# Performance work log

Measured on AMD Instinct MI355X. Metric: run time of the kernel, lower is better.

Reference implementation:

```python
import jax, jax.numpy as jnp
import numpy as np
from jax import lax

V, E, NL, NS, DC, EX = 32000, 1024, 4, 16, 4, 2
DI = EX * E          # 2048 inner dim
DTR = E // 16        # 64 dt_rank
BSZ, L = 2, 512
EPS = 1e-5


def setup_inputs() -> dict:
    key = jax.random.key(0)
    ks = jax.random.split(key, 12)
    s = 0.02
    emb = jax.random.normal(ks[0], (V, E), jnp.float32) * s
    ln_w = jnp.ones((NL, E), jnp.float32)
    ln_b = jnp.zeros((NL, E), jnp.float32)
    in_proj_w = jax.random.normal(ks[1], (NL, 2 * DI, E), jnp.float32) * s
    conv_w = jax.random.normal(ks[2], (NL, DI, DC), jnp.float32) * 0.1
    conv_b = jnp.zeros((NL, DI), jnp.float32)
    x_proj_w = jax.random.normal(ks[3], (NL, DTR + 2 * NS, DI), jnp.float32) * s
    dt_proj_w = jax.random.normal(ks[4], (NL, DI, DTR), jnp.float32) * s
    dt_proj_b = jax.random.normal(ks[5], (NL, DI), jnp.float32) * 0.1
    # canonical S4D-real init: A[d,n] = n+1  ->  A_log = log(A)
    A_log = jnp.log(jnp.tile(jnp.arange(1, NS + 1, dtype=jnp.float32)[None, None, :], (NL, DI, 1)))
    D_param = jnp.ones((NL, DI), jnp.float32)
    out_proj_w = jax.random.normal(ks[6], (NL, E, DI), jnp.float32) * s
    fln_w = jnp.ones((E,), jnp.float32)
    fln_b = jnp.zeros((E,), jnp.float32)
    input_ids = jax.random.randint(ks[7], (BSZ, L), 0, V, jnp.int64)
    targets = jax.random.randint(ks[8], (BSZ, L), 0, V, jnp.int64)
    return dict(input_ids=input_ids, targets=targets, emb=emb, ln_w=ln_w, ln_b=ln_b,
                in_proj_w=in_proj_w, conv_w=conv_w, conv_b=conv_b, x_proj_w=x_proj_w,
                dt_proj_w=dt_proj_w, dt_proj_b=dt_proj_b, A_log=A_log, D_param=D_param,
                out_proj_w=out_proj_w, fln_w=fln_w, fln_b=fln_b)


def _layer_norm(x, w, b):
    mu = x.mean(-1, keepdims=True)
    var = ((x - mu) ** 2).mean(-1, keepdims=True)
    return (x - mu) * lax.rsqrt(var + EPS) * w + b


def _mamba_block(x, in_w, cw, cb, xw, dtw, dtb, a_log, d_par, ow):
    # x: (B,L,E)
    xz = jnp.einsum('ble,fe->blf', x, in_w)          # (B,L,2*DI)
    u, res = jnp.split(xz, 2, axis=-1)               # each (B,L,DI)
    # causal depthwise conv1d, kernel width DC (left pad DC-1)
    u_pad = jnp.pad(u, ((0, 0), (DC - 1, 0), (0, 0)))
    u_conv = sum(cw[:, k] * u_pad[:, k:k + u.shape[1], :] for k in range(DC))
    u = jax.nn.silu(u_conv + cb)
    x_dbl = jnp.einsum('bld,fd->blf', u, xw)         # (B,L,DTR+2*NS)
    dt = x_dbl[..., :DTR]
    Bm = x_dbl[..., DTR:DTR + NS]                    # (B,L,NS)
    Cm = x_dbl[..., DTR + NS:]                       # (B,L,NS)
    delta = jax.nn.softplus(jnp.einsum('blr,dr->bld', dt, dtw) + dtb)  # (B,L,DI)
    A = -jnp.exp(a_log)                              # (DI,NS)
    dA = jnp.exp(delta[..., None] * A)               # (B,L,DI,NS)
    dBu = delta[..., None] * Bm[:, :, None, :] * u[..., None]

    def step(h, inp):
        dA_t, dBu_t, C_t = inp
        h = dA_t * h + dBu_t                         # (B,DI,NS)
        y = jnp.einsum('bdn,bn->bd', h, C_t)
        return h, y

    h0 = jnp.zeros((x.shape[0], DI, NS), x.dtype)
    _, ys = lax.scan(step, h0, (dA.transpose(1, 0, 2, 3), dBu.transpose(1, 0, 2, 3), Cm.transpose(1, 0, 2)))
    y = ys.transpose(1, 0, 2) + u * d_par            # (B,L,DI)
    y = y * jax.nn.silu(res)
    return jnp.einsum('bld,ed->ble', y, ow)


def reference(input_ids, targets, emb, ln_w, ln_b, in_proj_w, conv_w, conv_b,
              x_proj_w, dt_proj_w, dt_proj_b, A_log, D_param, out_proj_w, fln_w, fln_b):
    x = emb[input_ids]                               # (B,L,E)
    for l in range(NL):
        h = _layer_norm(x, ln_w[l], ln_b[l])
        h = _mamba_block(h, in_proj_w[l], conv_w[l], conv_b[l], x_proj_w[l],
                         dt_proj_w[l], dt_proj_b[l], A_log[l], D_param[l], out_proj_w[l])
        x = x + h
    x = _layer_norm(x, fln_w, fln_b)
    logits = jnp.einsum('ble,ve->blv', x, emb)       # tied lm_head
    logp = jax.nn.log_softmax(logits, axis=-1)
    valid = targets != -1
    safe_t = jnp.where(valid, targets, 0)
    nll = -jnp.take_along_axis(logp, safe_t[..., None], axis=-1)[..., 0]
    loss = jnp.where(valid, nll, 0.0).mean()
    return logits, loss
```

## Files before the change

### kernel.cpp

```cpp
#include <hip/hip_runtime.h>
#include <cstdint>
#include <cstddef>

#define L_SEQ 512
#define NBATCH 2
#define NTOK 1024
#define E_DIM 1024
#define V_DIM 32000
#define DI_DIM 2048
#define NS_DIM 16
#define DTR_DIM 64
#define DC_DIM 4
#define NL_DIM 4
#define NC 8
#define LC (L_SEQ / NC)
#define CB_LOG 250

typedef __bf16 bf16;
typedef __bf16 bf16x8 __attribute__((ext_vector_type(8)));
typedef __bf16 bf16x4 __attribute__((ext_vector_type(4)));
typedef float  f32x4  __attribute__((ext_vector_type(4)));

__device__ __forceinline__ void gload_lds16(const void* g, void* l)
{
    __builtin_amdgcn_global_load_lds((const __attribute__((address_space(1))) uint32_t*)g,
                                     (__attribute__((address_space(3))) uint32_t*)l, 16, 0, 0);
}

__device__ __forceinline__ float softplusf(float z)
{
    return fmaxf(z, 0.0f) + log1pf(expf(-fabsf(z)));
}

__global__ void cast_f32_to_bf16(const float* __restrict__ in, bf16* __restrict__ out, int n4)
{
    int stride = gridDim.x * blockDim.x;
    for (int i = blockIdx.x * blockDim.x + threadIdx.x; i < n4; i += stride) {
        f32x4 v = ((const f32x4*)in)[i];
        bf16x4 o;
        o[0] = (bf16)v[0]; o[1] = (bf16)v[1]; o[2] = (bf16)v[2]; o[3] = (bf16)v[3];
        ((bf16x4*)out)[i] = o;
    }
}

__global__ void cast3_kernel(const float* __restrict__ a, bf16* __restrict__ oa, int na4,
                             const float* __restrict__ b, bf16* __restrict__ ob, int nb4,
                             const float* __restrict__ c, bf16* __restrict__ oc, int nc4)
{
    int stride = gridDim.x * blockDim.x;
    int tot = na4 + nb4 + nc4;
    for (int i = blockIdx.x * blockDim.x + threadIdx.x; i < tot; i += stride) {
        const float* src; bf16* dst; int k = i;
        if (k < na4) { src = a; dst = oa; }
        else if ((k -= na4) < nb4) { src = b; dst = ob; }
        else { k -= nb4; src = c; dst = oc; }
        f32x4 v = ((const f32x4*)src)[k];
        bf16x4 o;
        o[0] = (bf16)v[0]; o[1] = (bf16)v[1]; o[2] = (bf16)v[2]; o[3] = (bf16)v[3];
        ((bf16x4*)dst)[k] = o;
    }
}

__global__ void embed_kernel(const int* __restrict__ ids, const float* __restrict__ emb,
                             float* __restrict__ x)
{
    int t = blockIdx.x;
    int id = ids[t];
    ((f32x4*)(x + (size_t)t * E_DIM))[threadIdx.x] =
        ((const f32x4*)(emb + (size_t)id * E_DIM))[threadIdx.x];
}

__global__ void ln_kernel(const float* __restrict__ x, const float* __restrict__ w,
                          const float* __restrict__ b, bf16* __restrict__ out)
{
    int t = blockIdx.x;
    int tid = threadIdx.x;
    f32x4 v = ((const f32x4*)(x + (size_t)t * E_DIM))[tid];
    float s  = v[0] + v[1] + v[2] + v[3];
    float sq = v[0]*v[0] + v[1]*v[1] + v[2]*v[2] + v[3]*v[3];
#pragma unroll
    for (int off = 1; off < 64; off <<= 1) { s += __shfl_xor(s, off); sq += __shfl_xor(sq, off); }
    __shared__ float ps[4], pq[4];
    if ((tid & 63) == 0) { ps[tid >> 6] = s; pq[tid >> 6] = sq; }
    __syncthreads();
    float S  = ps[0] + ps[1] + ps[2] + ps[3];
    float SQ = pq[0] + pq[1] + pq[2] + pq[3];
    float mu  = S * (1.0f / E_DIM);
    float var = SQ * (1.0f / E_DIM) - mu * mu;
    float rs  = rsqrtf(var + 1e-5f);
    f32x4 wv = ((const f32x4*)w)[tid];
    f32x4 bv = ((const f32x4*)b)[tid];
    bf16x4 o;
#pragma unroll
    for (int i = 0; i < 4; ++i) o[i] = (bf16)((v[i] - mu) * rs * wv[i] + bv[i]);
    ((bf16x4*)(out + (size_t)t * E_DIM))[tid] = o;
}

template<int BM, int BN, int MODE>
__global__ __launch_bounds__(256) void gemm_bt(const bf16* __restrict__ A, const bf16* __restrict__ B,
                                               void* __restrict__ Cv, int K,
                                               int lda, int ldb, int ldc,
                                               const float* __restrict__ bias,
                                               float* __restrict__ Pm, float* __restrict__ Ps,
                                               int RB, int CB, int CBpad)
{
    int pid = blockIdx.x;
    int xcd = pid & 7;
    int j   = pid >> 3;
    int cpx = CBpad >> 3;
    int rb  = j % RB;
    int cb  = xcd * cpx + j / RB;
    if (cb >= CB) return;

    __shared__ __align__(16) bf16 As[BM * 32];
    __shared__ __align__(16) bf16 Bs[BN * 32];
    int tid  = threadIdx.x;
    int lane = tid & 63;
    int wid  = tid >> 6;
    int wr = wid >> 1, wc = wid & 1;
    int li = lane & 15, lg = lane >> 4;
    const bf16* Ablk = A + (size_t)(rb * BM) * lda;
    const bf16* Bblk = B + (size_t)(cb * BN) * ldb;
    constexpr int MR  = BM / 32;
    constexpr int NR  = BN / 32;
    constexpr int TOT = (BM + BN) * 4;
    f32x4 acc[MR][NR] = {};
    for (int k0 = 0; k0 < K; k0 += 32) {
        __syncthreads();
#pragma unroll
        for (int it = 0; it < TOT / 256; ++it) {
            int wbase = it * 256 + wid * 64;
            int idx   = wbase + lane;
            if (wbase < BM * 4) {
                int row = idx >> 2, seg = idx & 3;
                gload_lds16(Ablk + (size_t)row * lda + k0 + seg * 8, As + (size_t)wbase * 8);
            } else {
                int bb  = wbase - BM * 4;
                int bi  = bb + lane;
                int row = bi >> 2, seg = bi & 3;
                gload_lds16(Bblk + (size_t)row * ldb + k0 + seg * 8, Bs + (size_t)bb * 8);
            }
        }
        __syncthreads();
        bf16x8 af[MR], bfr[NR];
#pragma unroll
        for (int m = 0; m < MR; ++m) af[m]  = *(const bf16x8*)&As[(wr * (BM/2) + m * 16 + li) * 32 + lg * 8];
#pragma unroll
        for (int n = 0; n < NR; ++n) bfr[n] = *(const bf16x8*)&Bs[(wc * (BN/2) + n * 16 + li) * 32 + lg * 8];
#pragma unroll
        for (int m = 0; m < MR; ++m)
#pragma unroll
            for (int n = 0; n < NR; ++n)
                acc[m][n] = __builtin_amdgcn_mfma_f32_16x16x32_bf16(af[m], bfr[n], acc[m][n], 0, 0, 0);
    }
    int row0 = rb * BM + wr * (BM/2);
    int col0 = cb * BN + wc * (BN/2);
    float* Cf = (float*)Cv;
    bf16*  Cb = (bf16*)Cv;
#pragma unroll
    for (int m = 0; m < MR; ++m) {
#pragma unroll
        for (int n = 0; n < NR; ++n) {
            int r = row0 + m * 16 + lg * 4;
            int c = col0 + n * 16 + li;
#pragma unroll
            for (int q = 0; q < 4; ++q) {
                float v = acc[m][n][q];
                if (MODE == 0 || MODE == 3) {
                    Cf[(size_t)(r + q) * ldc + c] = v;
                } else if (MODE == 1) {
                    float* cp = Cf + (size_t)(r + q) * ldc + c;
                    *cp = v + *cp;
                } else if (MODE == 2) {
                    Cb[(size_t)(r + q) * ldc + c] = (bf16)softplusf(v + bias[c]);
                } else if (MODE == 4) {
                    Cb[(size_t)(r + q) * ldc + c] = (bf16)v;
                }
            }
        }
    }
    if constexpr (MODE == 3) {
#pragma unroll
        for (int m = 0; m < MR; ++m) {
#pragma unroll
            for (int q = 0; q < 4; ++q) {
                float mx = acc[m][0][q];
#pragma unroll
                for (int n = 1; n < NR; ++n) mx = fmaxf(mx, acc[m][n][q]);
#pragma unroll
                for (int off = 1; off < 16; off <<= 1) mx = fmaxf(mx, __shfl_xor(mx, off));
                float sv = 0.0f;
#pragma unroll
                for (int n = 0; n < NR; ++n) sv += __expf(acc[m][n][q] - mx);
#pragma unroll
                for (int off = 1; off < 16; off <<= 1) sv += __shfl_xor(sv, off);
                if (li == 0) {
                    size_t r = (size_t)(row0 + m * 16 + lg * 4 + q);
                    Pm[r * 512 + cb * 2 + wc] = mx;
                    Ps[r * 512 + cb * 2 + wc] = sv;
                }
            }
        }
    }
}

template<int BM, int BN, int MODE>
static void launch_gemm(const bf16* A, const bf16* B, void* C, int M, int N, int K,
                        int lda, int ldb, int ldc, const float* bias,
                        float* Pm, float* Ps, hipStream_t stream)
{
    int RB = M / BM;
    int CB = (N + BN - 1) / BN;
    int CBpad = (CB + 7) & ~7;
    gemm_bt<BM, BN, MODE><<<RB * CBpad, 256, 0, stream>>>(A, B, C, K, lda, ldb, ldc,
                                                          bias, Pm, Ps, RB, CB, CBpad);
}

__global__ __launch_bounds__(256) void cxk_kernel(
        const bf16* __restrict__ xz, const float* __restrict__ cw,
        const float* __restrict__ cb, const float* __restrict__ xw,
        float* __restrict__ xdbl, bf16* __restrict__ dt_bf, bf16* __restrict__ u_bf)
{
    int t0  = blockIdx.x * 4;
    int bb  = t0 >> 9;
    int tid = threadIdx.x;
    int f   = tid & 127;
    int ks  = tid >> 7;
    __shared__ __align__(16) float sxz[7][256];
    __shared__ __align__(16) float su[4][256];
    __shared__ float pacc[4][128];
    float acc[4] = {0, 0, 0, 0};
    for (int kc = 0; kc < DI_DIM; kc += 256) {
        __syncthreads();
        if (tid < 224) {
            int row = tid >> 5, c8 = (tid & 31) * 8;
            int tr = t0 - 3 + row;
            float vals[8] = {0, 0, 0, 0, 0, 0, 0, 0};
            if (tr >= bb * L_SEQ) {
                bf16x8 v = *(const bf16x8*)&xz[(size_t)tr * (2 * DI_DIM) + kc + c8];
#pragma unroll
                for (int jj = 0; jj < 8; ++jj) vals[jj] = (float)v[jj];
            }
#pragma unroll
            for (int jj = 0; jj < 8; ++jj) sxz[row][c8 + jj] = vals[jj];
        }
        __syncthreads();
        {
            int c = tid;
            const float* cwp = cw + (size_t)(kc + c) * DC_DIM;
            float w0 = cwp[0], w1 = cwp[1], w2 = cwp[2], w3 = cwp[3];
            float bs = cb[kc + c];
#pragma unroll
            for (int tt = 0; tt < 4; ++tt) {
                float a = bs + w0 * sxz[tt][c] + w1 * sxz[tt + 1][c]
                             + w2 * sxz[tt + 2][c] + w3 * sxz[tt + 3][c];
                float uo = a / (1.0f + __expf(-a));
                su[tt][c] = uo;
                u_bf[(size_t)(t0 + tt) * DI_DIM + kc + c] = (bf16)uo;
            }
        }
        __syncthreads();
        if (f < 96) {
            int kb = ks * 128;
            for (int kk = kb; kk < kb + 128; kk += 4) {
                f32x4 wv = *(const f32x4*)&xw[(size_t)f * DI_DIM + kc + kk];
#pragma unroll
                for (int tt = 0; tt < 4; ++tt) {
                    f32x4 uv = *(f32x4*)&su[tt][kk];
                    acc[tt] += wv[0]*uv[0] + wv[1]*uv[1] + wv[2]*uv[2] + wv[3]*uv[3];
                }
            }
        }
    }
    if (ks == 1 && f < 96) {
#pragma unroll
        for (int tt = 0; tt < 4; ++tt) pacc[tt][f] = acc[tt];
    }
    __syncthreads();
    if (ks == 0 && f < 96) {
#pragma unroll
        for (int tt = 0; tt < 4; ++tt) {
            float v = acc[tt] + pacc[tt][f];
            xdbl[(size_t)(t0 + tt) * 96 + f] = v;
            if (f < 64) dt_bf[(size_t)(t0 + tt) * DTR_DIM + f] = (bf16)v;
        }
    }
}

__global__ __launch_bounds__(256) void scan_phase_a(
        const bf16* __restrict__ delta, const float* __restrict__ xdbl,
        const bf16* __restrict__ u_bf, const float* __restrict__ A_log,
        float* __restrict__ Pbuf, float* __restrict__ Sbuf)
{
    int tid = threadIdx.x;
    int c   = blockIdx.x & (NC - 1);
    int dblk= (blockIdx.x >> 3) & 127;
    int b   = blockIdx.x >> 10;
    int d0  = dblk << 4;
    int n = tid & 15, dl = tid >> 4;
    int d = d0 + dl;
    float Ac = -expf(A_log[(size_t)d * NS_DIM + n]);
    float h = 0.0f, P = 1.0f;
    __shared__ float s_dlt[32][16], s_u[32][16], s_B[32][16];
    int tt0 = tid >> 4, cc = tid & 15;
    int tbase = b * L_SEQ + c * LC;
    for (int t0 = 0; t0 < LC; t0 += 32) {
        __syncthreads();
#pragma unroll
        for (int jj = 0; jj < 2; ++jj) {
            int tt = jj * 16 + tt0;
            size_t trow = (size_t)(tbase + t0 + tt);
            s_dlt[tt][cc] = (float)delta[trow * DI_DIM + d0 + cc];
            s_u[tt][cc]   = (float)u_bf[trow * DI_DIM + d0 + cc];
            s_B[tt][cc]   = xdbl[trow * 96 + 64 + cc];
        }
        __syncthreads();
#pragma unroll
        for (int t = 0; t < 32; ++t) {
            float dlt = s_dlt[t][dl];
            float dA  = __expf(dlt * Ac);
            h = fmaf(dA, h, dlt * s_B[t][n] * s_u[t][dl]);
            P *= dA;
        }
    }
    size_t oi = (((size_t)(b * NC + c) * DI_DIM) + d) * NS_DIM + n;
    Pbuf[oi] = P;
    Sbuf[oi] = h;
}

__global__ void scan_combine(const float* __restrict__ Pbuf, const float* __restrict__ Sbuf,
                             float* __restrict__ Hstart)
{
    int i  = blockIdx.x * 256 + threadIdx.x;
    int b  = i >> 15;
    int dn = i & 32767;
    float h = 0.0f;
#pragma unroll
    for (int c = 0; c < NC; ++c) {
        size_t oi = ((size_t)(b * NC + c) * (DI_DIM * NS_DIM)) + dn;
        Hstart[oi] = h;
        h = fmaf(Pbuf[oi], h, Sbuf[oi]);
    }
}

__global__ __launch_bounds__(256) void scan_phase_c(
        const bf16* __restrict__ delta, const float* __restrict__ xdbl,
        const bf16* __restrict__ u_bf, const bf16* __restrict__ xz,
        const float* __restrict__ A_log, const float* __restrict__ D_par,
        const float* __restrict__ Hstart, bf16* __restrict__ y)
{
    int tid = threadIdx.x;
    int c   = blockIdx.x & (NC - 1);
    int dblk= (blockIdx.x >> 3) & 127;
    int b   = blockIdx.x >> 10;
    int d0  = dblk << 4;
    int n = tid & 15, dl = tid >> 4;
    int d = d0 + dl;
    float Ac = -expf(A_log[(size_t)d * NS_DIM + n]);
    float Dp = D_par[d];
    float h = Hstart[(((size_t)(b * NC + c) * DI_DIM) + d) * NS_DIM + n];
    __shared__ float s_dlt[32][16], s_u[32][16], s_res[32][16], s_B[32][16], s_C[32][16];
    __shared__ bf16  s_y[32][16];
    int tt0 = tid >> 4, cc = tid & 15;
    int tbase = b * L_SEQ + c * LC;
    for (int t0 = 0; t0 < LC; t0 += 32) {
        __syncthreads();
#pragma unroll
        for (int jj = 0; jj < 2; ++jj) {
            int tt = jj * 16 + tt0;
            size_t trow = (size_t)(tbase + t0 + tt);
            s_dlt[tt][cc] = (float)delta[trow * DI_DIM + d0 + cc];
            s_u[tt][cc]   = (float)u_bf[trow * DI_DIM + d0 + cc];
            s_res[tt][cc] = (float)xz[trow * (2 * DI_DIM) + DI_DIM + d0 + cc];
            s_B[tt][cc]   = xdbl[trow * 96 + 64 + cc];
            s_C[tt][cc]   = xdbl[trow * 96 + 80 + cc];
        }
        __syncthreads();
#pragma unroll
        for (int t = 0; t < 32; ++t) {
            float dlt = s_dlt[t][dl];
            float uu  = s_u[t][dl];
            float dA  = __expf(dlt * Ac);
            float dBu = dlt * s_B[t][n] * uu;
            h = fmaf(dA, h, dBu);
            float yp = h * s_C[t][n];
            yp += __shfl_xor(yp, 1);
            yp += __shfl_xor(yp, 2);
            yp += __shfl_xor(yp, 4);
            yp += __shfl_xor(yp, 8);
            if (n == 0) {
                float res = s_res[t][dl];
                float yv  = fmaf(uu, Dp, yp) * (res / (1.0f + __expf(-res)));
                s_y[t][dl] = (bf16)yv;
            }
        }
        __syncthreads();
#pragma unroll
        for (int jj = 0; jj < 2; ++jj) {
            int tt = jj * 16 + tt0;
            size_t trow = (size_t)(tbase + t0 + tt);
            y[trow * DI_DIM + d0 + cc] = s_y[tt][cc];
        }
    }
}

__global__ void lse_fin_kernel(const float* __restrict__ Pm, const float* __restrict__ Ps,
                               const float* __restrict__ logits, const int* __restrict__ targets,
                               float* __restrict__ lossp)
{
    int t = blockIdx.x, tid = threadIdx.x;
    float m = -1e30f, s = 0.0f;
    for (int i = tid; i < 2 * CB_LOG; i += 256) {
        float mo = Pm[(size_t)t * 512 + i], so = Ps[(size_t)t * 512 + i];
        float nm = fmaxf(m, mo);
        s = s * __expf(m - nm) + so * __expf(mo - nm);
        m = nm;
    }
#pragma unroll
    for (int off = 1; off < 64; off <<= 1) {
        float mo = __shfl_xor(m, off), so = __shfl_xor(s, off);
        float nm = fmaxf(m, mo);
        s = s * __expf(m - nm) + so * __expf(mo - nm);
        m = nm;
    }
    __shared__ float pm[4], ps2[4];
    if ((tid & 63) == 0) { pm[tid >> 6] = m; ps2[tid >> 6] = s; }
    __syncthreads();
    if (tid == 0) {
        float M = fmaxf(fmaxf(pm[0], pm[1]), fmaxf(pm[2], pm[3]));
        float S = ps2[0] * __expf(pm[0] - M) + ps2[1] * __expf(pm[1] - M)
                + ps2[2] * __expf(pm[2] - M) + ps2[3] * __expf(pm[3] - M);
        int tg = targets[t];
        if (tg >= 0) {
            float v = (M + logf(S)) - logits[(size_t)t * V_DIM + tg];
            atomicAdd(lossp, v * (1.0f / NTOK));
        }
    }
}

extern "C" void kernel_launch(void* const* d_in, const int* in_sizes, int n_in,
                              void* d_out, int out_size, void* d_ws, size_t ws_size,
                              hipStream_t stream)
{
    const int*   ids   = (const int*)d_in[0];
    const int*   tgt   = (const int*)d_in[1];
    const float* emb   = (const float*)d_in[2];
    const float* ln_w  = (const float*)d_in[3];
    const float* ln_b  = (const float*)d_in[4];
    const float* inw   = (const float*)d_in[5];
    const float* convw = (const float*)d_in[6];
    const float* convb = (const float*)d_in[7];
    const float* xw    = (const float*)d_in[8];
    const float* dtw   = (const float*)d_in[9];
    const float* dtb   = (const float*)d_in[10];
    const float* alog  = (const float*)d_in[11];
    const float* dpar  = (const float*)d_in[12];
    const float* outw  = (const float*)d_in[13];
    const float* flnw  = (const float*)d_in[14];
    const float* flnb  = (const float*)d_in[15];
    float* logits = (float*)d_out;
    float* lossp  = logits + (size_t)NTOK * V_DIM;

    char* wsp = (char*)d_ws;
    size_t off = 0;
    auto alloc = [&](size_t bytes) -> void* {
        void* p = wsp + off;
        off += (bytes + 255) & ~(size_t)255;
        return p;
    };
    bf16*  emb_bf  = (bf16*)alloc((size_t)V_DIM * E_DIM * 2);
    bf16*  winl    = (bf16*)alloc((size_t)2 * DI_DIM * E_DIM * 2);
    bf16*  woutl   = (bf16*)alloc((size_t)E_DIM * DI_DIM * 2);
    bf16*  wdtl    = (bf16*)alloc((size_t)DI_DIM * DTR_DIM * 2);
    float* x       = (float*)alloc((size_t)NTOK * E_DIM * 4);
    bf16*  h_bf    = (bf16*)alloc((size_t)NTOK * E_DIM * 2);
    bf16*  xzb     = (bf16*)alloc((size_t)NTOK * 2 * DI_DIM * 2);
    bf16*  u_bf    = (bf16*)alloc((size_t)NTOK * DI_DIM * 2);
    float* xdbl    = (float*)alloc((size_t)NTOK * 96 * 4);
    bf16*  dt_bf   = (bf16*)alloc((size_t)NTOK * DTR_DIM * 2);
    bf16*  deltab  = (bf16*)alloc((size_t)NTOK * DI_DIM * 2);
    bf16*  y_bf    = (bf16*)alloc((size_t)NTOK * DI_DIM * 2);
    bf16*  xf_bf   = (bf16*)alloc((size_t)NTOK * E_DIM * 2);
    float* Pbuf    = (float*)alloc((size_t)NBATCH * NC * DI_DIM * NS_DIM * 4);
    float* Sbuf    = (float*)alloc((size_t)NBATCH * NC * DI_DIM * NS_DIM * 4);
    float* Hstart  = (float*)alloc((size_t)NBATCH * NC * DI_DIM * NS_DIM * 4);
    float* Pm      = (float*)alloc((size_t)NTOK * 512 * 4);
    float* Ps      = (float*)alloc((size_t)NTOK * 512 * 4);
    if (off > ws_size) return;

    hipMemsetAsync(lossp, 0, sizeof(float), stream);
    {
        int n4 = (int)((size_t)V_DIM * E_DIM / 4);
        cast_f32_to_bf16<<<4096, 256, 0, stream>>>(emb, emb_bf, n4);
    }
    embed_kernel<<<NTOK, 256, 0, stream>>>(ids, emb, x);

    for (int l = 0; l < NL_DIM; ++l) {
        cast3_kernel<<<2048, 256, 0, stream>>>(
            inw  + (size_t)l * 2 * DI_DIM * E_DIM, winl,  (int)((size_t)2 * DI_DIM * E_DIM / 4),
            outw + (size_t)l * E_DIM * DI_DIM,     woutl, (int)((size_t)E_DIM * DI_DIM / 4),
            dtw  + (size_t)l * DI_DIM * DTR_DIM,   wdtl,  (int)((size_t)DI_DIM * DTR_DIM / 4));

        ln_kernel<<<NTOK, 256, 0, stream>>>(x, ln_w + l * E_DIM, ln_b + l * E_DIM, h_bf);
        launch_gemm<128, 64, 4>(h_bf, winl, xzb, NTOK, 2 * DI_DIM, E_DIM,
                                E_DIM, E_DIM, 2 * DI_DIM, nullptr, nullptr, nullptr, stream);
        cxk_kernel<<<NTOK / 4, 256, 0, stream>>>(
            xzb, convw + (size_t)l * DI_DIM * DC_DIM, convb + (size_t)l * DI_DIM,
            xw + (size_t)l * 96 * DI_DIM, xdbl, dt_bf, u_bf);
        launch_gemm<64, 64, 2>(dt_bf, wdtl, deltab, NTOK, DI_DIM, DTR_DIM,
                               DTR_DIM, DTR_DIM, DI_DIM, dtb + (size_t)l * DI_DIM,
                               nullptr, nullptr, stream);
        scan_phase_a<<<NBATCH * (DI_DIM / 16) * NC, 256, 0, stream>>>(
            deltab, xdbl, u_bf, alog + (size_t)l * DI_DIM * NS_DIM, Pbuf, Sbuf);
        scan_combine<<<NBATCH * DI_DIM * NS_DIM / 256, 256, 0, stream>>>(Pbuf, Sbuf, Hstart);
        scan_phase_c<<<NBATCH * (DI_DIM / 16) * NC, 256, 0, stream>>>(
            deltab, xdbl, u_bf, xzb, alog + (size_t)l * DI_DIM * NS_DIM,
            dpar + (size_t)l * DI_DIM, Hstart, y_bf);
        launch_gemm<64, 64, 1>(y_bf, woutl, x, NTOK, E_DIM, DI_DIM,
                               DI_DIM, DI_DIM, E_DIM, nullptr, nullptr, nullptr, stream);
    }
    ln_kernel<<<NTOK, 256, 0, stream>>>(x, flnw, flnb, xf_bf);
    launch_gemm<128, 128, 3>(xf_bf, emb_bf, logits, NTOK, V_DIM, E_DIM,
                             E_DIM, E_DIM, V_DIM, nullptr, Pm, Ps, stream);
    lse_fin_kernel<<<NTOK, 256, 0, stream>>>(Pm, Ps, logits, tgt, lossp);
}
```

Measured before the change: 884.9 us.

## Unfuse softmax partials from LM-head GEMM and halve tokens per conv block

```diff
diff --git a/kernel.cpp b/kernel.cpp
--- a/kernel.cpp
+++ b/kernel.cpp
@@ -14,7 +14,6 @@
 #define NL_DIM 4
 #define NC 8
 #define LC (L_SEQ / NC)
-#define CB_LOG 250
 
 typedef __bf16 bf16;
 typedef __bf16 bf16x8 __attribute__((ext_vector_type(8)));
@@ -101,7 +100,6 @@
                                                void* __restrict__ Cv, int K,
                                                int lda, int ldb, int ldc,
                                                const float* __restrict__ bias,
-                                               float* __restrict__ Pm, float* __restrict__ Ps,
                                                int RB, int CB, int CBpad)
 {
     int pid = blockIdx.x;
@@ -166,7 +164,7 @@
 #pragma unroll
             for (int q = 0; q < 4; ++q) {
                 float v = acc[m][n][q];
-                if (MODE == 0 || MODE == 3) {
+                if (MODE == 0) {
                     Cf[(size_t)(r + q) * ldc + c] = v;
                 } else if (MODE == 1) {
                     float* cp = Cf + (size_t)(r + q) * ldc + c;
@@ -179,41 +177,17 @@
             }
         }
     }
-    if constexpr (MODE == 3) {
-#pragma unroll
-        for (int m = 0; m < MR; ++m) {
-#pragma unroll
-            for (int q = 0; q < 4; ++q) {
-                float mx = acc[m][0][q];
-#pragma unroll
-                for (int n = 1; n < NR; ++n) mx = fmaxf(mx, acc[m][n][q]);
-#pragma unroll
-                for (int off = 1; off < 16; off <<= 1) mx = fmaxf(mx, __shfl_xor(mx, off));
-                float sv = 0.0f;
-#pragma unroll
-                for (int n = 0; n < NR; ++n) sv += __expf(acc[m][n][q] - mx);
-#pragma unroll
-                for (int off = 1; off < 16; off <<= 1) sv += __shfl_xor(sv, off);
-                if (li == 0) {
-                    size_t r = (size_t)(row0 + m * 16 + lg * 4 + q);
-                    Pm[r * 512 + cb * 2 + wc] = mx;
-                    Ps[r * 512 + cb * 2 + wc] = sv;
-                }
-            }
-        }
-    }
 }
 
 template<int BM, int BN, int MODE>
 static void launch_gemm(const bf16* A, const bf16* B, void* C, int M, int N, int K,
-                        int lda, int ldb, int ldc, const float* bias,
-                        float* Pm, float* Ps, hipStream_t stream)
+                        int lda, int ldb, int ldc, const float* bias, hipStream_t stream)
 {
     int RB = M / BM;
     int CB = (N + BN - 1) / BN;
     int CBpad = (CB + 7) & ~7;
     gemm_bt<BM, BN, MODE><<<RB * CBpad, 256, 0, stream>>>(A, B, C, K, lda, ldb, ldc,
-                                                          bias, Pm, Ps, RB, CB, CBpad);
+                                                          bias, RB, CB, CBpad);
 }
 
 __global__ __launch_bounds__(256) void cxk_kernel(
@@ -221,28 +195,31 @@
         const float* __restrict__ cb, const float* __restrict__ xw,
         float* __restrict__ xdbl, bf16* __restrict__ dt_bf, bf16* __restrict__ u_bf)
 {
-    int t0  = blockIdx.x * 4;
+    int t0  = blockIdx.x * 2;
     int bb  = t0 >> 9;
     int tid = threadIdx.x;
     int f   = tid & 127;
     int ks  = tid >> 7;
-    __shared__ __align__(16) float sxz[7][256];
-    __shared__ __align__(16) float su[4][256];
-    __shared__ float pacc[4][128];
-    float acc[4] = {0, 0, 0, 0};
+    __shared__ __align__(16) float sxz[5][256];
+    __shared__ __align__(16) float su[2][256];
+    __shared__ float pacc[2][128];
+    float acc[2] = {0, 0};
     for (int kc = 0; kc < DI_DIM; kc += 256) {
         __syncthreads();
-        if (tid < 224) {
-            int row = tid >> 5, c8 = (tid & 31) * 8;
-            int tr = t0 - 3 + row;
-            float vals[8] = {0, 0, 0, 0, 0, 0, 0, 0};
-            if (tr >= bb * L_SEQ) {
-                bf16x8 v = *(const bf16x8*)&xz[(size_t)tr * (2 * DI_DIM) + kc + c8];
-#pragma unroll
-                for (int jj = 0; jj < 8; ++jj) vals[jj] = (float)v[jj];
+#pragma unroll
+        for (int it = 0; it < 2; ++it) {
+            int idx = it * 256 + tid;
+            if (idx < 320) {
+                int row = idx >> 6, c4 = (idx & 63) * 4;
+                int tr = t0 - 3 + row;
+                float v0 = 0, v1 = 0, v2 = 0, v3 = 0;
+                if (tr >= bb * L_SEQ) {
+                    bf16x4 v = *(const bf16x4*)&xz[(size_t)tr * (2 * DI_DIM) + kc + c4];
+                    v0 = (float)v[0]; v1 = (float)v[1]; v2 = (float)v[2]; v3 = (float)v[3];
+                }
+                sxz[row][c4] = v0; sxz[row][c4 + 1] = v1;
+                sxz[row][c4 + 2] = v2; sxz[row][c4 + 3] = v3;
             }
-#pragma unroll
-            for (int jj = 0; jj < 8; ++jj) sxz[row][c8 + jj] = vals[jj];
         }
         __syncthreads();
         {
@@ -251,7 +228,7 @@
             float w0 = cwp[0], w1 = cwp[1], w2 = cwp[2], w3 = cwp[3];
             float bs = cb[kc + c];
 #pragma unroll
-            for (int tt = 0; tt < 4; ++tt) {
+            for (int tt = 0; tt < 2; ++tt) {
                 float a = bs + w0 * sxz[tt][c] + w1 * sxz[tt + 1][c]
                              + w2 * sxz[tt + 2][c] + w3 * sxz[tt + 3][c];
                 float uo = a / (1.0f + __expf(-a));
@@ -265,7 +242,7 @@
             for (int kk = kb; kk < kb + 128; kk += 4) {
                 f32x4 wv = *(const f32x4*)&xw[(size_t)f * DI_DIM + kc + kk];
 #pragma unroll
-                for (int tt = 0; tt < 4; ++tt) {
+                for (int tt = 0; tt < 2; ++tt) {
                     f32x4 uv = *(f32x4*)&su[tt][kk];
                     acc[tt] += wv[0]*uv[0] + wv[1]*uv[1] + wv[2]*uv[2] + wv[3]*uv[3];
                 }
@@ -274,12 +251,12 @@
     }
     if (ks == 1 && f < 96) {
 #pragma unroll
-        for (int tt = 0; tt < 4; ++tt) pacc[tt][f] = acc[tt];
+        for (int tt = 0; tt < 2; ++tt) pacc[tt][f] = acc[tt];
     }
     __syncthreads();
     if (ks == 0 && f < 96) {
 #pragma unroll
-        for (int tt = 0; tt < 4; ++tt) {
+        for (int tt = 0; tt < 2; ++tt) {
             float v = acc[tt] + pacc[tt][f];
             xdbl[(size_t)(t0 + tt) * 96 + f] = v;
             if (f < 64) dt_bf[(size_t)(t0 + tt) * DTR_DIM + f] = (bf16)v;
@@ -404,17 +381,17 @@
     }
 }
 
-__global__ void lse_fin_kernel(const float* __restrict__ Pm, const float* __restrict__ Ps,
-                               const float* __restrict__ logits, const int* __restrict__ targets,
+__global__ void lse_nll_kernel(const float* __restrict__ logits, const int* __restrict__ targets,
                                float* __restrict__ lossp)
 {
     int t = blockIdx.x, tid = threadIdx.x;
+    const f32x4* row = (const f32x4*)(logits + (size_t)t * V_DIM);
     float m = -1e30f, s = 0.0f;
-    for (int i = tid; i < 2 * CB_LOG; i += 256) {
-        float mo = Pm[(size_t)t * 512 + i], so = Ps[(size_t)t * 512 + i];
-        float nm = fmaxf(m, mo);
-        s = s * __expf(m - nm) + so * __expf(mo - nm);
-        m = nm;
+    for (int i = tid; i < V_DIM / 4; i += 256) {
+        f32x4 v = row[i];
+        float m4 = fmaxf(fmaxf(v[0], v[1]), fmaxf(v[2], v[3]));
+        if (m4 > m) { s *= __expf(m - m4); m = m4; }
+        s += __expf(v[0] - m) + __expf(v[1] - m) + __expf(v[2] - m) + __expf(v[3] - m);
     }
 #pragma unroll
     for (int off = 1; off < 64; off <<= 1) {
@@ -484,8 +461,6 @@
     float* Pbuf    = (float*)alloc((size_t)NBATCH * NC * DI_DIM * NS_DIM * 4);
     float* Sbuf    = (float*)alloc((size_t)NBATCH * NC * DI_DIM * NS_DIM * 4);
     float* Hstart  = (float*)alloc((size_t)NBATCH * NC * DI_DIM * NS_DIM * 4);
-    float* Pm      = (float*)alloc((size_t)NTOK * 512 * 4);
-    float* Ps      = (float*)alloc((size_t)NTOK * 512 * 4);
     if (off > ws_size) return;
 
     hipMemsetAsync(lossp, 0, sizeof(float), stream);
@@ -503,13 +478,12 @@
 
         ln_kernel<<<NTOK, 256, 0, stream>>>(x, ln_w + l * E_DIM, ln_b + l * E_DIM, h_bf);
         launch_gemm<128, 64, 4>(h_bf, winl, xzb, NTOK, 2 * DI_DIM, E_DIM,
-                                E_DIM, E_DIM, 2 * DI_DIM, nullptr, nullptr, nullptr, stream);
-        cxk_kernel<<<NTOK / 4, 256, 0, stream>>>(
+                                E_DIM, E_DIM, 2 * DI_DIM, nullptr, stream);
+        cxk_kernel<<<NTOK / 2, 256, 0, stream>>>(
             xzb, convw + (size_t)l * DI_DIM * DC_DIM, convb + (size_t)l * DI_DIM,
             xw + (size_t)l * 96 * DI_DIM, xdbl, dt_bf, u_bf);
         launch_gemm<64, 64, 2>(dt_bf, wdtl, deltab, NTOK, DI_DIM, DTR_DIM,
-                               DTR_DIM, DTR_DIM, DI_DIM, dtb + (size_t)l * DI_DIM,
-                               nullptr, nullptr, stream);
+                               DTR_DIM, DTR_DIM, DI_DIM, dtb + (size_t)l * DI_DIM, stream);
         scan_phase_a<<<NBATCH * (DI_DIM / 16) * NC, 256, 0, stream>>>(
             deltab, xdbl, u_bf, alog + (size_t)l * DI_DIM * NS_DIM, Pbuf, Sbuf);
         scan_combine<<<NBATCH * DI_DIM * NS_DIM / 256, 256, 0, stream>>>(Pbuf, Sbuf, Hstart);
@@ -517,10 +491,10 @@
             deltab, xdbl, u_bf, xzb, alog + (size_t)l * DI_DIM * NS_DIM,
             dpar + (size_t)l * DI_DIM, Hstart, y_bf);
         launch_gemm<64, 64, 1>(y_bf, woutl, x, NTOK, E_DIM, DI_DIM,
-                               DI_DIM, DI_DIM, E_DIM, nullptr, nullptr, nullptr, stream);
+                               DI_DIM, DI_DIM, E_DIM, nullptr, stream);
     }
     ln_kernel<<<NTOK, 256, 0, stream>>>(x, flnw, flnb, xf_bf);
-    launch_gemm<128, 128, 3>(xf_bf, emb_bf, logits, NTOK, V_DIM, E_DIM,
-                             E_DIM, E_DIM, V_DIM, nullptr, Pm, Ps, stream);
-    lse_fin_kernel<<<NTOK, 256, 0, stream>>>(Pm, Ps, logits, tgt, lossp);
-}
+    launch_gemm<128, 128, 0>(xf_bf, emb_bf, logits, NTOK, V_DIM, E_DIM,
+                             E_DIM, E_DIM, V_DIM, nullptr, stream);
+    lse_nll_kernel<<<NTOK, 256, 0, stream>>>(logits, tgt, lossp);
+}
```

New measurement: 921.5 us. 1.04x slower.
